# Kernel tuning notes

Hardware: AMD Instinct MI355X
Metric: run time of the kernel (lower is better)

The kernel has to match this reference:

```python
import jax, jax.numpy as jnp
import numpy as np

HIDDEN = 2048
HEAD_SIZE = 8
EXTRA = 4
NH = HEAD_SIZE * EXTRA          # 32 effective heads
D = HIDDEN // (HEAD_SIZE * 16)  # 16 per-head dim
PROJ = NH * D                   # 512
# NOTE: the torch module scales by att_size**-0.5 where att_size is the
# PRE-division value hidden//head_size//4 = 64, not the per-head dim D=16.
SCALE = (HIDDEN // HEAD_SIZE // EXTRA) ** -0.5


def _xavier(key, out_dim, in_dim):
    bound = float(np.sqrt(6.0 / (in_dim + out_dim)))
    return jax.random.uniform(key, (out_dim, in_dim), jnp.float32, -bound, bound)


def setup_inputs() -> dict:
    key = jax.random.key(0)
    ks = jax.random.split(key, 7)
    B, S = 2, 2048
    return {
        "q": jax.random.normal(ks[0], (B, S, HIDDEN), jnp.float32),
        "k": jax.random.normal(ks[1], (B, S, HIDDEN), jnp.float32),
        "v": jax.random.normal(ks[2], (B, S, HIDDEN), jnp.float32),
        "Wq": _xavier(ks[3], PROJ, HIDDEN),
        "Wk": _xavier(ks[4], PROJ, HIDDEN),
        "Wv": _xavier(ks[5], PROJ, HIDDEN),
        "Wo": _xavier(ks[6], HIDDEN, PROJ),
    }


def reference(q, k, v, Wq, Wk, Wv, Wo):
    B, S, _ = q.shape
    # projections (torch Linear: x @ W.T), reshape to [B,S,heads,d]
    qh = (q @ Wq.T).reshape(B, S, NH, D)
    kh = (k @ Wk.T).reshape(B, S, NH, D)
    vh = (v @ Wv.T).reshape(B, S, NH, D)
    scores = jnp.einsum("bshd,bthd->bhst", qh * SCALE, kh)  # [B,NH,S,S]
    attn = jax.nn.softmax(scores, axis=-1)
    out = jnp.einsum("bhst,bthd->bshd", attn, vh).reshape(B, S, PROJ)
    return out @ Wo.T  # [B,S,HIDDEN]
```

## Files before the change

kernel.cpp:

```cpp
#include <hip/hip_runtime.h>

#define HIDDEN 2048
#define NH 32
#define HD 16
#define PROJ 512
#define SEQ 2048

using f32x4    = __attribute__((ext_vector_type(4))) float;
using f32x2    = __attribute__((ext_vector_type(2))) float;
using bf16x8   = __attribute__((ext_vector_type(8))) __bf16;

__device__ __forceinline__ unsigned short f2bf(float x) {
  unsigned int u = __float_as_uint(x);
  u += 0x7FFFu + ((u >> 16) & 1u);
  return (unsigned short)(u >> 16);
}

__device__ __forceinline__ f32x4 mfma_bf16(bf16x8 a, bf16x8 b, f32x4 c) {
  return __builtin_amdgcn_mfma_f32_16x16x32_bf16(a, b, c, 0, 0, 0);
}

__device__ __forceinline__ f32x2 pk_add(f32x2 a, f32x2 b) {
  f32x2 d;
  asm("v_pk_add_f32 %0, %1, %2" : "=v"(d) : "v"(a), "v"(b));
  return d;
}

__device__ __forceinline__ unsigned int cvt_pk_bf16(float lo, float hi) {
  unsigned int d;
  asm("v_cvt_pk_bf16_f32 %0, %1, %2" : "=v"(d) : "v"(lo), "v"(hi));
  return d;
}

#define GLDS16(gptr, lptr)                                              \
  __builtin_amdgcn_global_load_lds(                                     \
      (const __attribute__((address_space(1))) unsigned int*)(gptr),    \
      (__attribute__((address_space(3))) unsigned int*)(lptr), 16, 0, 0)

__global__ __launch_bounds__(256)
void conv_kernel(const float* __restrict__ q, const float* __restrict__ k,
                 const float* __restrict__ v,
                 const float* __restrict__ Wq, const float* __restrict__ Wk,
                 const float* __restrict__ Wv, const float* __restrict__ Wo,
                 unsigned short* __restrict__ qb, unsigned short* __restrict__ kb,
                 unsigned short* __restrict__ vb,
                 unsigned short* __restrict__ Wqb, unsigned short* __restrict__ Wkb,
                 unsigned short* __restrict__ Wvb, unsigned short* __restrict__ Wob) {
  const int bid = blockIdx.x;
  const float* src;
  unsigned short* dst;
  size_t i;
  if (bid < 24576) {
    const int z = bid >> 13;
    const int off = bid & 8191;
    src = (z == 0) ? q : (z == 1) ? k : v;
    dst = (z == 0) ? qb : (z == 1) ? kb : vb;
    i = ((size_t)off * 256 + threadIdx.x) * 4;
  } else {
    const int r = bid - 24576;
    const int z = r >> 10;
    const int off = r & 1023;
    src = (z == 0) ? Wq : (z == 1) ? Wk : (z == 2) ? Wv : Wo;
    dst = (z == 0) ? Wqb : (z == 1) ? Wkb : (z == 2) ? Wvb : Wob;
    i = ((size_t)off * 256 + threadIdx.x) * 4;
  }
  f32x4 x = *(const f32x4*)(src + i);
  uint2 p;
  p.x = f2bf(x[0]) | ((unsigned)f2bf(x[1]) << 16);
  p.y = f2bf(x[2]) | ((unsigned)f2bf(x[3]) << 16);
  *(uint2*)(dst + i) = p;
}

__global__ __launch_bounds__(256)
void proj_kernel(const unsigned short* __restrict__ qb,
                 const unsigned short* __restrict__ kb,
                 const unsigned short* __restrict__ vb,
                 const unsigned short* __restrict__ Wqb,
                 const unsigned short* __restrict__ Wkb,
                 const unsigned short* __restrict__ Wvb,
                 unsigned short* __restrict__ qh, unsigned short* __restrict__ kh,
                 unsigned short* __restrict__ vt) {
  const int lin = blockIdx.x;
  const int e = lin & 7;
  const int t = lin >> 3;
  const int colt = t & 3;
  const int j = t >> 2;
  const int y = e + 8 * j;
  const int z = y >> 6;
  const int row0 = (y & 63) * 64;
  const int col0 = colt * 128;

  const unsigned short* A = (z == 0) ? qb : (z == 1) ? kb : vb;
  const unsigned short* Wb = (z == 0) ? Wqb : (z == 1) ? Wkb : Wvb;
  const float scale = (z == 0) ? 0.18033688011112042f  : 1.0f;

  __shared__ unsigned short As[64 * 32];
  __shared__ unsigned short Bs[128 * 32];

  const int tid = threadIdx.x;
  const int w = tid >> 6;
  const int lane = tid & 63;
  const int ln = lane & 15;
  const int qd = lane >> 4;
  const int wm = w >> 1, wn = w & 1;

  const int aM = tid >> 2;
  const int aG = (tid & 3) ^ (aM & 3);
  int bN[2], bG[2];
#pragma unroll
  for (int s = 0; s < 2; s++) {
    int L = s * 256 + tid;
    bN[s] = L >> 2;
    bG[s] = (L & 3) ^ (bN[s] & 3);
  }

  f32x4 acc[2][4];
#pragma unroll
  for (int mi = 0; mi < 2; mi++)
#pragma unroll
    for (int ni = 0; ni < 4; ni++) acc[mi][ni] = (f32x4){0.f, 0.f, 0.f, 0.f};

  for (int k0 = 0; k0 < HIDDEN; k0 += 32) {
    GLDS16(A + (size_t)(row0 + aM) * HIDDEN + k0 + aG * 8, &As[tid * 8]);
#pragma unroll
    for (int s = 0; s < 2; s++)
      GLDS16(Wb + (size_t)(col0 + bN[s]) * HIDDEN + k0 + bG[s] * 8,
             &Bs[(s * 256 + tid) * 8]);
    __syncthreads();

    bf16x8 af[2], bfv[4];
#pragma unroll
    for (int mi = 0; mi < 2; mi++) {
      int m = wm * 32 + mi * 16 + ln;
      af[mi] = *(const bf16x8*)&As[(m * 4 + (qd ^ (m & 3))) * 8];
    }
#pragma unroll
    for (int ni = 0; ni < 4; ni++) {
      int n = wn * 64 + ni * 16 + ln;
      bfv[ni] = *(const bf16x8*)&Bs[(n * 4 + (qd ^ (n & 3))) * 8];
    }
#pragma unroll
    for (int mi = 0; mi < 2; mi++)
#pragma unroll
      for (int ni = 0; ni < 4; ni++)
        acc[mi][ni] = mfma_bf16(af[mi], bfv[ni], acc[mi][ni]);
    __syncthreads();
  }

  if (z == 2) {
#pragma unroll
    for (int mi = 0; mi < 2; mi++)
#pragma unroll
      for (int ni = 0; ni < 4; ni++) {
        int h = (col0 + wn * 64 + ni * 16) >> 4;
        int grow0 = row0 + wm * 32 + mi * 16 + qd * 4;
        int b = grow0 >> 11, s0 = grow0 & 2047;
        uint2 o2;
        o2.x = f2bf(acc[mi][ni][0]) | ((unsigned)f2bf(acc[mi][ni][1]) << 16);
        o2.y = f2bf(acc[mi][ni][2]) | ((unsigned)f2bf(acc[mi][ni][3]) << 16);
        *(uint2*)&vt[((size_t)(b * NH + h) * HD + ln) * SEQ + s0] = o2;
      }
  } else {
    unsigned short* out = (z == 0) ? qh : kh;
#pragma unroll
    for (int mi = 0; mi < 2; mi++)
#pragma unroll
      for (int ni = 0; ni < 4; ni++) {
        int h = (col0 + wn * 64 + ni * 16) >> 4;
#pragma unroll
        for (int r = 0; r < 4; r++) {
          int grow = row0 + wm * 32 + mi * 16 + qd * 4 + r;
          int b = grow >> 11, s = grow & 2047;
          out[((size_t)(b * NH + h) * SEQ + s) * HD + ln] = f2bf(acc[mi][ni][r] * scale);
        }
      }
  }
}

__global__ __launch_bounds__(256, 4)
void flash_kernel(const unsigned short* __restrict__ qh,
                  const unsigned short* __restrict__ kh,
                  const unsigned short* __restrict__ vt,
                  unsigned short* __restrict__ attnb) {
  const int bh = blockIdx.x;
  const int b = bh >> 5, h = bh & 31;
  const int q0 = blockIdx.y * 128;
  const size_t hoff = (size_t)bh * SEQ * HD;
  const unsigned short* Qp = qh + hoff;
  const unsigned short* Kp = kh + hoff;
  const unsigned short* Vth = vt + hoff;

  __shared__ unsigned short Qs[128 * 16];
  __shared__ unsigned short Ks[2][128 * 16];
  __shared__ unsigned short Vts[2][256 * 8];
  __shared__ unsigned short Ps[4][32 * 40];
  __shared__ __align__(16) unsigned short Zz[8];

  const int tid = threadIdx.x;
  const int w = tid >> 6;
  const int lane = tid & 63;
  const int ln = lane & 15;
  const int qd = lane >> 4;
  const bool hiq = (qd >= 2);

  if (tid < 8) Zz[tid] = 0;

  const int vD = tid >> 4;
  const int vG = (tid & 15) ^ vD;

  const int qkOff = (tid >> 1) * 16 + (((tid & 1) ^ ((tid >> 3) & 1)) * 8);
  const int hsel = ((qd & 1) ^ ((ln >> 2) & 1)) * 8;

  GLDS16(Qp + (size_t)q0 * HD + qkOff, &Qs[tid * 8]);
  GLDS16(Kp + qkOff, &Ks[0][tid * 8]);
  GLDS16(Vth + (size_t)vD * SEQ + vG * 8, &Vts[0][tid * 8]);
  __syncthreads();

  bf16x8 aq[2];
#pragma unroll
  for (int ni = 0; ni < 2; ni++) {
    const unsigned short* src =
        hiq ? Zz : &Qs[(w * 32 + ni * 16 + ln) * 16 + hsel];
    aq[ni] = *(const bf16x8*)src;
  }

  f32x2 lsum2[2] = {{0.f, 0.f}, {0.f, 0.f}};
  f32x4 o_acc[2] = {{0.f, 0.f, 0.f, 0.f}, {0.f, 0.f, 0.f, 0.f}};
  unsigned short* Pw = &Ps[w][0];

  for (int t = 0; t < 16; t++) {
    const int buf = t & 1;
    if (t < 15) {
      GLDS16(Kp + (size_t)(t + 1) * 2048 + qkOff, &Ks[buf ^ 1][tid * 8]);
      GLDS16(Vth + (size_t)vD * SEQ + (t + 1) * 128 + vG * 8, &Vts[buf ^ 1][tid * 8]);
    }
    const unsigned short* Kb = &Ks[buf][0];
    const unsigned short* Vb = &Vts[buf][0];

#pragma unroll
    for (int c = 0; c < 4; c++) {
      f32x4 sc[2][2];
#pragma unroll
      for (int hf = 0; hf < 2; hf++) {
        int tile = c * 2 + hf;
        const unsigned short* asrc =
            hiq ? Zz : &Kb[(tile * 16 + ln) * 16 + hsel];
        bf16x8 ak = *(const bf16x8*)asrc;
#pragma unroll
        for (int ni = 0; ni < 2; ni++)
          sc[ni][hf] = mfma_bf16(ak, aq[ni], (f32x4){0.f, 0.f, 0.f, 0.f});
      }
      bf16x8 av = *(const bf16x8*)&Vb[(ln * 16 + ((c * 4 + qd) ^ ln)) * 8];

#pragma unroll
      for (int ni = 0; ni < 2; ni++) {
        float e0 = __builtin_amdgcn_exp2f(sc[ni][0][0]);
        float e1 = __builtin_amdgcn_exp2f(sc[ni][0][1]);
        float e2 = __builtin_amdgcn_exp2f(sc[ni][0][2]);
        float e3 = __builtin_amdgcn_exp2f(sc[ni][0][3]);
        float e4 = __builtin_amdgcn_exp2f(sc[ni][1][0]);
        float e5 = __builtin_amdgcn_exp2f(sc[ni][1][1]);
        float e6 = __builtin_amdgcn_exp2f(sc[ni][1][2]);
        float e7 = __builtin_amdgcn_exp2f(sc[ni][1][3]);
        f32x2 s01 = pk_add((f32x2){e0, e1}, (f32x2){e2, e3});
        f32x2 s23 = pk_add((f32x2){e4, e5}, (f32x2){e6, e7});
        lsum2[ni] = pk_add(lsum2[ni], pk_add(s01, s23));
        unsigned int d0 = cvt_pk_bf16(e0, e1);
        unsigned int d1 = cvt_pk_bf16(e2, e3);
        unsigned int d2 = cvt_pk_bf16(e4, e5);
        unsigned int d3 = cvt_pk_bf16(e6, e7);
        *(uint2*)&Pw[(ni * 16 + ln) * 40 + qd * 4] = make_uint2(d0, d1);
        *(uint2*)&Pw[(ni * 16 + ln) * 40 + 16 + qd * 4] = make_uint2(d2, d3);
      }

#pragma unroll
      for (int ni = 0; ni < 2; ni++) {
        bf16x8 bp = *(const bf16x8*)&Pw[(ni * 16 + ln) * 40 + qd * 8];
        o_acc[ni] = mfma_bf16(av, bp, o_acc[ni]);
      }
    }
    __syncthreads();
  }

#pragma unroll
  for (int ni = 0; ni < 2; ni++) {
    float l = lsum2[ni][0] + lsum2[ni][1];
    l += __shfl_xor(l, 16, 64);
    l += __shfl_xor(l, 32, 64);
    float invl = 1.0f / l;
    int s = q0 + w * 32 + ni * 16 + ln;
    f32x4 res = o_acc[ni] * invl;
    uint2 o2;
    o2.x = f2bf(res[0]) | ((unsigned)f2bf(res[1]) << 16);
    o2.y = f2bf(res[2]) | ((unsigned)f2bf(res[3]) << 16);
    *(uint2*)&attnb[((size_t)(b * SEQ + s)) * PROJ + h * HD + qd * 4] = o2;
  }
}

__global__ __launch_bounds__(256)
void out_kernel(const unsigned short* __restrict__ attnb,
                const unsigned short* __restrict__ Wob,
                float* __restrict__ out) {
  const int lin = blockIdx.x;
  const int e = lin & 7;
  const int t = lin >> 3;
  const int col0 = (e * 2 + (t & 1)) * 128;
  const int row0 = (t >> 1) * 64;

  __shared__ unsigned short As[64 * 32];
  __shared__ unsigned short Bs[128 * 32];

  const int tid = threadIdx.x;
  const int w = tid >> 6;
  const int lane = tid & 63;
  const int ln = lane & 15;
  const int qd = lane >> 4;
  const int wm = w >> 1, wn = w & 1;

  const int aM = tid >> 2;
  const int aG = (tid & 3) ^ (aM & 3);
  int bN[2], bG[2];
#pragma unroll
  for (int s = 0; s < 2; s++) {
    int L = s * 256 + tid;
    bN[s] = L >> 2;
    bG[s] = (L & 3) ^ (bN[s] & 3);
  }

  f32x4 acc[2][4];
#pragma unroll
  for (int mi = 0; mi < 2; mi++)
#pragma unroll
    for (int ni = 0; ni < 4; ni++) acc[mi][ni] = (f32x4){0.f, 0.f, 0.f, 0.f};

  for (int k0 = 0; k0 < PROJ; k0 += 32) {
    GLDS16(attnb + (size_t)(row0 + aM) * PROJ + k0 + aG * 8, &As[tid * 8]);
#pragma unroll
    for (int s = 0; s < 2; s++)
      GLDS16(Wob + (size_t)(col0 + bN[s]) * PROJ + k0 + bG[s] * 8,
             &Bs[(s * 256 + tid) * 8]);
    __syncthreads();

    bf16x8 af[2], bfv[4];
#pragma unroll
    for (int mi = 0; mi < 2; mi++) {
      int m = wm * 32 + mi * 16 + ln;
      af[mi] = *(const bf16x8*)&As[(m * 4 + (qd ^ (m & 3))) * 8];
    }
#pragma unroll
    for (int ni = 0; ni < 4; ni++) {
      int n = wn * 64 + ni * 16 + ln;
      bfv[ni] = *(const bf16x8*)&Bs[(n * 4 + (qd ^ (n & 3))) * 8];
    }
#pragma unroll
    for (int mi = 0; mi < 2; mi++)
#pragma unroll
      for (int ni = 0; ni < 4; ni++)
        acc[mi][ni] = mfma_bf16(bfv[ni], af[mi], acc[mi][ni]);
    __syncthreads();
  }

#pragma unroll
  for (int mi = 0; mi < 2; mi++) {
    int grow = row0 + wm * 32 + mi * 16 + ln;
#pragma unroll
    for (int ni = 0; ni < 4; ni++) {
      int gcol = col0 + wn * 64 + ni * 16 + qd * 4;
      *(f32x4*)&out[(size_t)grow * HIDDEN + gcol] = acc[mi][ni];
    }
  }
}

extern "C" void kernel_launch(void* const* d_in, const int* in_sizes, int n_in,
                              void* d_out, int out_size, void* d_ws, size_t ws_size,
                              hipStream_t stream) {
  const float* q  = (const float*)d_in[0];
  const float* k  = (const float*)d_in[1];
  const float* v  = (const float*)d_in[2];
  const float* Wq = (const float*)d_in[3];
  const float* Wk = (const float*)d_in[4];
  const float* Wv = (const float*)d_in[5];
  const float* Wo = (const float*)d_in[6];

  char* ws = (char*)d_ws;
  const size_t MB = 1024 * 1024;
  unsigned short* qh    = (unsigned short*)(ws);
  unsigned short* kh    = (unsigned short*)(ws + 4 * MB);
  unsigned short* vt    = (unsigned short*)(ws + 8 * MB);
  unsigned short* attnb = (unsigned short*)(ws + 12 * MB);
  unsigned short* Wqb   = (unsigned short*)(ws + 16 * MB);
  unsigned short* Wkb   = (unsigned short*)(ws + 18 * MB);
  unsigned short* Wvb   = (unsigned short*)(ws + 20 * MB);
  unsigned short* Wob   = (unsigned short*)(ws + 22 * MB);
  unsigned short* qb    = (unsigned short*)(ws + 24 * MB);
  unsigned short* kb    = (unsigned short*)(ws + 40 * MB);
  unsigned short* vb    = (unsigned short*)(ws + 56 * MB);

  conv_kernel<<<dim3(28672), dim3(256), 0, stream>>>(q, k, v, Wq, Wk, Wv, Wo,
                                                     qb, kb, vb, Wqb, Wkb, Wvb, Wob);
  proj_kernel<<<dim3(768), dim3(256), 0, stream>>>(qb, kb, vb, Wqb, Wkb, Wvb, qh, kh, vt);
  flash_kernel<<<dim3(64, 16), dim3(256), 0, stream>>>(qh, kh, vt, attnb);
  out_kernel<<<dim3(1024), dim3(256), 0, stream>>>(attnb, Wob, (float*)d_out);

  (void)in_sizes; (void)n_in; (void)out_size; (void)ws_size;
}
```

Baseline: 266.6 us.

## Fuse fp32-to-bf16 conversion into projection and output GEMM loads

Drops the separate conversion kernel. The projection and output GEMMs now load fp32 inputs and weights into registers, convert them to bf16 with v_cvt_pk_bf16, and store to LDS. The next K-slice is prefetched into registers after the barrier. The output GEMM tile also grows from 64 to 128 rows, halving its grid and reusing each Wo tile twice. This removes a full read and write of bf16 copies of q/k/v, but the main GEMM loop now reads twice the bytes from global memory, and LDS writes are synchronous rather than async global-to-LDS.

```diff
diff --git a/kernel.cpp b/kernel.cpp
--- a/kernel.cpp
+++ b/kernel.cpp
@@ -38,46 +38,10 @@
       (__attribute__((address_space(3))) unsigned int*)(lptr), 16, 0, 0)
 
 __global__ __launch_bounds__(256)
-void conv_kernel(const float* __restrict__ q, const float* __restrict__ k,
+void proj_kernel(const float* __restrict__ q, const float* __restrict__ k,
                  const float* __restrict__ v,
                  const float* __restrict__ Wq, const float* __restrict__ Wk,
-                 const float* __restrict__ Wv, const float* __restrict__ Wo,
-                 unsigned short* __restrict__ qb, unsigned short* __restrict__ kb,
-                 unsigned short* __restrict__ vb,
-                 unsigned short* __restrict__ Wqb, unsigned short* __restrict__ Wkb,
-                 unsigned short* __restrict__ Wvb, unsigned short* __restrict__ Wob) {
-  const int bid = blockIdx.x;
-  const float* src;
-  unsigned short* dst;
-  size_t i;
-  if (bid < 24576) {
-    const int z = bid >> 13;
-    const int off = bid & 8191;
-    src = (z == 0) ? q : (z == 1) ? k : v;
-    dst = (z == 0) ? qb : (z == 1) ? kb : vb;
-    i = ((size_t)off * 256 + threadIdx.x) * 4;
-  } else {
-    const int r = bid - 24576;
-    const int z = r >> 10;
-    const int off = r & 1023;
-    src = (z == 0) ? Wq : (z == 1) ? Wk : (z == 2) ? Wv : Wo;
-    dst = (z == 0) ? Wqb : (z == 1) ? Wkb : (z == 2) ? Wvb : Wob;
-    i = ((size_t)off * 256 + threadIdx.x) * 4;
-  }
-  f32x4 x = *(const f32x4*)(src + i);
-  uint2 p;
-  p.x = f2bf(x[0]) | ((unsigned)f2bf(x[1]) << 16);
-  p.y = f2bf(x[2]) | ((unsigned)f2bf(x[3]) << 16);
-  *(uint2*)(dst + i) = p;
-}
-
-__global__ __launch_bounds__(256)
-void proj_kernel(const unsigned short* __restrict__ qb,
-                 const unsigned short* __restrict__ kb,
-                 const unsigned short* __restrict__ vb,
-                 const unsigned short* __restrict__ Wqb,
-                 const unsigned short* __restrict__ Wkb,
-                 const unsigned short* __restrict__ Wvb,
+                 const float* __restrict__ Wv,
                  unsigned short* __restrict__ qh, unsigned short* __restrict__ kh,
                  unsigned short* __restrict__ vt) {
   const int lin = blockIdx.x;
@@ -90,8 +54,8 @@
   const int row0 = (y & 63) * 64;
   const int col0 = colt * 128;
 
-  const unsigned short* A = (z == 0) ? qb : (z == 1) ? kb : vb;
-  const unsigned short* Wb = (z == 0) ? Wqb : (z == 1) ? Wkb : Wvb;
+  const float* A = (z == 0) ? q : (z == 1) ? k : v;
+  const float* Wb = (z == 0) ? Wq : (z == 1) ? Wk : Wv;
   const float scale = (z == 0) ? 0.18033688011112042f  : 1.0f;
 
   __shared__ unsigned short As[64 * 32];
@@ -114,19 +78,52 @@
     bG[s] = (L & 3) ^ (bN[s] & 3);
   }
 
+  const float* Aptr  = A + (size_t)(row0 + aM) * HIDDEN + aG * 8;
+  const float* Bptr0 = Wb + (size_t)(col0 + bN[0]) * HIDDEN + bG[0] * 8;
+  const float* Bptr1 = Wb + (size_t)(col0 + bN[1]) * HIDDEN + bG[1] * 8;
+
   f32x4 acc[2][4];
 #pragma unroll
   for (int mi = 0; mi < 2; mi++)
 #pragma unroll
     for (int ni = 0; ni < 4; ni++) acc[mi][ni] = (f32x4){0.f, 0.f, 0.f, 0.f};
 
+  f32x4 ra0 = *(const f32x4*)(Aptr);
+  f32x4 ra1 = *(const f32x4*)(Aptr + 4);
+  f32x4 rb00 = *(const f32x4*)(Bptr0);
+  f32x4 rb01 = *(const f32x4*)(Bptr0 + 4);
+  f32x4 rb10 = *(const f32x4*)(Bptr1);
+  f32x4 rb11 = *(const f32x4*)(Bptr1 + 4);
+
   for (int k0 = 0; k0 < HIDDEN; k0 += 32) {
-    GLDS16(A + (size_t)(row0 + aM) * HIDDEN + k0 + aG * 8, &As[tid * 8]);
-#pragma unroll
-    for (int s = 0; s < 2; s++)
-      GLDS16(Wb + (size_t)(col0 + bN[s]) * HIDDEN + k0 + bG[s] * 8,
-             &Bs[(s * 256 + tid) * 8]);
+    uint4 wa;
+    wa.x = cvt_pk_bf16(ra0[0], ra0[1]);
+    wa.y = cvt_pk_bf16(ra0[2], ra0[3]);
+    wa.z = cvt_pk_bf16(ra1[0], ra1[1]);
+    wa.w = cvt_pk_bf16(ra1[2], ra1[3]);
+    *(uint4*)&As[tid * 8] = wa;
+    uint4 wb0;
+    wb0.x = cvt_pk_bf16(rb00[0], rb00[1]);
+    wb0.y = cvt_pk_bf16(rb00[2], rb00[3]);
+    wb0.z = cvt_pk_bf16(rb01[0], rb01[1]);
+    wb0.w = cvt_pk_bf16(rb01[2], rb01[3]);
+    *(uint4*)&Bs[tid * 8] = wb0;
+    uint4 wb1;
+    wb1.x = cvt_pk_bf16(rb10[0], rb10[1]);
+    wb1.y = cvt_pk_bf16(rb10[2], rb10[3]);
+    wb1.z = cvt_pk_bf16(rb11[0], rb11[1]);
+    wb1.w = cvt_pk_bf16(rb11[2], rb11[3]);
+    *(uint4*)&Bs[(256 + tid) * 8] = wb1;
     __syncthreads();
+
+    if (k0 + 32 < HIDDEN) {
+      ra0 = *(const f32x4*)(Aptr + k0 + 32);
+      ra1 = *(const f32x4*)(Aptr + k0 + 36);
+      rb00 = *(const f32x4*)(Bptr0 + k0 + 32);
+      rb01 = *(const f32x4*)(Bptr0 + k0 + 36);
+      rb10 = *(const f32x4*)(Bptr1 + k0 + 32);
+      rb11 = *(const f32x4*)(Bptr1 + k0 + 36);
+    }
 
     bf16x8 af[2], bfv[4];
 #pragma unroll
@@ -299,15 +296,15 @@
 
 __global__ __launch_bounds__(256)
 void out_kernel(const unsigned short* __restrict__ attnb,
-                const unsigned short* __restrict__ Wob,
+                const float* __restrict__ Wo,
                 float* __restrict__ out) {
   const int lin = blockIdx.x;
   const int e = lin & 7;
   const int t = lin >> 3;
   const int col0 = (e * 2 + (t & 1)) * 128;
-  const int row0 = (t >> 1) * 64;
-
-  __shared__ unsigned short As[64 * 32];
+  const int row0 = (t >> 1) * 128;
+
+  __shared__ unsigned short As[128 * 32];
   __shared__ unsigned short Bs[128 * 32];
 
   const int tid = threadIdx.x;
@@ -327,48 +324,80 @@
     bG[s] = (L & 3) ^ (bN[s] & 3);
   }
 
-  f32x4 acc[2][4];
-#pragma unroll
-  for (int mi = 0; mi < 2; mi++)
-#pragma unroll
-    for (int ni = 0; ni < 4; ni++) acc[mi][ni] = (f32x4){0.f, 0.f, 0.f, 0.f};
+  const float* Bptr0 = Wo + (size_t)(col0 + bN[0]) * PROJ + bG[0] * 8;
+  const float* Bptr1 = Wo + (size_t)(col0 + bN[1]) * PROJ + bG[1] * 8;
+
+  f32x4 acc[2][2][4];
+#pragma unroll
+  for (int s2 = 0; s2 < 2; s2++)
+#pragma unroll
+    for (int mi = 0; mi < 2; mi++)
+#pragma unroll
+      for (int ni = 0; ni < 4; ni++) acc[s2][mi][ni] = (f32x4){0.f, 0.f, 0.f, 0.f};
+
+  f32x4 rb00 = *(const f32x4*)(Bptr0);
+  f32x4 rb01 = *(const f32x4*)(Bptr0 + 4);
+  f32x4 rb10 = *(const f32x4*)(Bptr1);
+  f32x4 rb11 = *(const f32x4*)(Bptr1 + 4);
 
   for (int k0 = 0; k0 < PROJ; k0 += 32) {
     GLDS16(attnb + (size_t)(row0 + aM) * PROJ + k0 + aG * 8, &As[tid * 8]);
-#pragma unroll
-    for (int s = 0; s < 2; s++)
-      GLDS16(Wob + (size_t)(col0 + bN[s]) * PROJ + k0 + bG[s] * 8,
-             &Bs[(s * 256 + tid) * 8]);
+    GLDS16(attnb + (size_t)(row0 + 64 + aM) * PROJ + k0 + aG * 8, &As[(256 + tid) * 8]);
+    uint4 wb0;
+    wb0.x = cvt_pk_bf16(rb00[0], rb00[1]);
+    wb0.y = cvt_pk_bf16(rb00[2], rb00[3]);
+    wb0.z = cvt_pk_bf16(rb01[0], rb01[1]);
+    wb0.w = cvt_pk_bf16(rb01[2], rb01[3]);
+    *(uint4*)&Bs[tid * 8] = wb0;
+    uint4 wb1;
+    wb1.x = cvt_pk_bf16(rb10[0], rb10[1]);
+    wb1.y = cvt_pk_bf16(rb10[2], rb10[3]);
+    wb1.z = cvt_pk_bf16(rb11[0], rb11[1]);
+    wb1.w = cvt_pk_bf16(rb11[2], rb11[3]);
+    *(uint4*)&Bs[(256 + tid) * 8] = wb1;
     __syncthreads();
 
-    bf16x8 af[2], bfv[4];
-#pragma unroll
-    for (int mi = 0; mi < 2; mi++) {
-      int m = wm * 32 + mi * 16 + ln;
-      af[mi] = *(const bf16x8*)&As[(m * 4 + (qd ^ (m & 3))) * 8];
-    }
+    if (k0 + 32 < PROJ) {
+      rb00 = *(const f32x4*)(Bptr0 + k0 + 32);
+      rb01 = *(const f32x4*)(Bptr0 + k0 + 36);
+      rb10 = *(const f32x4*)(Bptr1 + k0 + 32);
+      rb11 = *(const f32x4*)(Bptr1 + k0 + 36);
+    }
+
+    bf16x8 af[2][2], bfv[4];
+#pragma unroll
+    for (int s2 = 0; s2 < 2; s2++)
+#pragma unroll
+      for (int mi = 0; mi < 2; mi++) {
+        int m = s2 * 64 + wm * 32 + mi * 16 + ln;
+        af[s2][mi] = *(const bf16x8*)&As[(m * 4 + (qd ^ (m & 3))) * 8];
+      }
 #pragma unroll
     for (int ni = 0; ni < 4; ni++) {
       int n = wn * 64 + ni * 16 + ln;
       bfv[ni] = *(const bf16x8*)&Bs[(n * 4 + (qd ^ (n & 3))) * 8];
     }
 #pragma unroll
-    for (int mi = 0; mi < 2; mi++)
-#pragma unroll
-      for (int ni = 0; ni < 4; ni++)
-        acc[mi][ni] = mfma_bf16(bfv[ni], af[mi], acc[mi][ni]);
+    for (int s2 = 0; s2 < 2; s2++)
+#pragma unroll
+      for (int mi = 0; mi < 2; mi++)
+#pragma unroll
+        for (int ni = 0; ni < 4; ni++)
+          acc[s2][mi][ni] = mfma_bf16(bfv[ni], af[s2][mi], acc[s2][mi][ni]);
     __syncthreads();
   }
 
 #pragma unroll
-  for (int mi = 0; mi < 2; mi++) {
-    int grow = row0 + wm * 32 + mi * 16 + ln;
-#pragma unroll
-    for (int ni = 0; ni < 4; ni++) {
-      int gcol = col0 + wn * 64 + ni * 16 + qd * 4;
-      *(f32x4*)&out[(size_t)grow * HIDDEN + gcol] = acc[mi][ni];
-    }
-  }
+  for (int s2 = 0; s2 < 2; s2++)
+#pragma unroll
+    for (int mi = 0; mi < 2; mi++) {
+      int grow = row0 + s2 * 64 + wm * 32 + mi * 16 + ln;
+#pragma unroll
+      for (int ni = 0; ni < 4; ni++) {
+        int gcol = col0 + wn * 64 + ni * 16 + qd * 4;
+        *(f32x4*)&out[(size_t)grow * HIDDEN + gcol] = acc[s2][mi][ni];
+      }
+    }
 }
 
 extern "C" void kernel_launch(void* const* d_in, const int* in_sizes, int n_in,
@@ -388,19 +417,10 @@
   unsigned short* kh    = (unsigned short*)(ws + 4 * MB);
   unsigned short* vt    = (unsigned short*)(ws + 8 * MB);
   unsigned short* attnb = (unsigned short*)(ws + 12 * MB);
-  unsigned short* Wqb   = (unsigned short*)(ws + 16 * MB);
-  unsigned short* Wkb   = (unsigned short*)(ws + 18 * MB);
-  unsigned short* Wvb   = (unsigned short*)(ws + 20 * MB);
-  unsigned short* Wob   = (unsigned short*)(ws + 22 * MB);
-  unsigned short* qb    = (unsigned short*)(ws + 24 * MB);
-  unsigned short* kb    = (unsigned short*)(ws + 40 * MB);
-  unsigned short* vb    = (unsigned short*)(ws + 56 * MB);
-
-  conv_kernel<<<dim3(28672), dim3(256), 0, stream>>>(q, k, v, Wq, Wk, Wv, Wo,
-                                                     qb, kb, vb, Wqb, Wkb, Wvb, Wob);
-  proj_kernel<<<dim3(768), dim3(256), 0, stream>>>(qb, kb, vb, Wqb, Wkb, Wvb, qh, kh, vt);
+
+  proj_kernel<<<dim3(768), dim3(256), 0, stream>>>(q, k, v, Wq, Wk, Wv, qh, kh, vt);
   flash_kernel<<<dim3(64, 16), dim3(256), 0, stream>>>(qh, kh, vt, attnb);
-  out_kernel<<<dim3(1024), dim3(256), 0, stream>>>(attnb, Wob, (float*)d_out);
+  out_kernel<<<dim3(512), dim3(256), 0, stream>>>(attnb, Wo, (float*)d_out);
 
   (void)in_sizes; (void)n_in; (void)out_size; (void)ws_size;
 }
```

Result: slower. 275.3 us (+3.3%).

## Double-buffer LDS tiles in projection and output GEMMs, enlarge output tile

Applied to the files above, without the earlier changes.

The projection and output GEMM kernels now hold two shared-memory buffers per operand. The next K-slice is prefetched while MFMAs run on the current slice, which overlaps global-to-LDS loads with compute and removes one barrier per iteration. The output kernel also doubles its row tile to 128, halving the grid to 512 blocks so each Wo tile loaded is reused across more rows. The cost is more LDS and more accumulator registers per block, which may lower occupancy.

```diff
diff --git a/kernel.cpp b/kernel.cpp
--- a/kernel.cpp
+++ b/kernel.cpp
@@ -94,8 +94,8 @@
   const unsigned short* Wb = (z == 0) ? Wqb : (z == 1) ? Wkb : Wvb;
   const float scale = (z == 0) ? 0.18033688011112042f  : 1.0f;
 
-  __shared__ unsigned short As[64 * 32];
-  __shared__ unsigned short Bs[128 * 32];
+  __shared__ unsigned short As[2][64 * 32];
+  __shared__ unsigned short Bs[2][128 * 32];
 
   const int tid = threadIdx.x;
   const int w = tid >> 6;
@@ -114,30 +114,39 @@
     bG[s] = (L & 3) ^ (bN[s] & 3);
   }
 
+  const unsigned short* Aptr  = A + (size_t)(row0 + aM) * HIDDEN + aG * 8;
+  const unsigned short* Bptr0 = Wb + (size_t)(col0 + bN[0]) * HIDDEN + bG[0] * 8;
+  const unsigned short* Bptr1 = Wb + (size_t)(col0 + bN[1]) * HIDDEN + bG[1] * 8;
+
   f32x4 acc[2][4];
 #pragma unroll
   for (int mi = 0; mi < 2; mi++)
 #pragma unroll
     for (int ni = 0; ni < 4; ni++) acc[mi][ni] = (f32x4){0.f, 0.f, 0.f, 0.f};
 
+  GLDS16(Aptr, &As[0][tid * 8]);
+  GLDS16(Bptr0, &Bs[0][tid * 8]);
+  GLDS16(Bptr1, &Bs[0][(256 + tid) * 8]);
+  __syncthreads();
+
   for (int k0 = 0; k0 < HIDDEN; k0 += 32) {
-    GLDS16(A + (size_t)(row0 + aM) * HIDDEN + k0 + aG * 8, &As[tid * 8]);
-#pragma unroll
-    for (int s = 0; s < 2; s++)
-      GLDS16(Wb + (size_t)(col0 + bN[s]) * HIDDEN + k0 + bG[s] * 8,
-             &Bs[(s * 256 + tid) * 8]);
-    __syncthreads();
+    const int cur = (k0 >> 5) & 1;
+    if (k0 + 32 < HIDDEN) {
+      GLDS16(Aptr + k0 + 32, &As[cur ^ 1][tid * 8]);
+      GLDS16(Bptr0 + k0 + 32, &Bs[cur ^ 1][tid * 8]);
+      GLDS16(Bptr1 + k0 + 32, &Bs[cur ^ 1][(256 + tid) * 8]);
+    }
 
     bf16x8 af[2], bfv[4];
 #pragma unroll
     for (int mi = 0; mi < 2; mi++) {
       int m = wm * 32 + mi * 16 + ln;
-      af[mi] = *(const bf16x8*)&As[(m * 4 + (qd ^ (m & 3))) * 8];
+      af[mi] = *(const bf16x8*)&As[cur][(m * 4 + (qd ^ (m & 3))) * 8];
     }
 #pragma unroll
     for (int ni = 0; ni < 4; ni++) {
       int n = wn * 64 + ni * 16 + ln;
-      bfv[ni] = *(const bf16x8*)&Bs[(n * 4 + (qd ^ (n & 3))) * 8];
+      bfv[ni] = *(const bf16x8*)&Bs[cur][(n * 4 + (qd ^ (n & 3))) * 8];
     }
 #pragma unroll
     for (int mi = 0; mi < 2; mi++)
@@ -305,10 +314,10 @@
   const int e = lin & 7;
   const int t = lin >> 3;
   const int col0 = (e * 2 + (t & 1)) * 128;
-  const int row0 = (t >> 1) * 64;
-
-  __shared__ unsigned short As[64 * 32];
-  __shared__ unsigned short Bs[128 * 32];
+  const int row0 = (t >> 1) * 128;
+
+  __shared__ unsigned short As[2][128 * 32];
+  __shared__ unsigned short Bs[2][128 * 32];
 
   const int tid = threadIdx.x;
   const int w = tid >> 6;
@@ -327,48 +336,68 @@
     bG[s] = (L & 3) ^ (bN[s] & 3);
   }
 
-  f32x4 acc[2][4];
-#pragma unroll
-  for (int mi = 0; mi < 2; mi++)
-#pragma unroll
-    for (int ni = 0; ni < 4; ni++) acc[mi][ni] = (f32x4){0.f, 0.f, 0.f, 0.f};
+  const unsigned short* Aptr0 = attnb + (size_t)(row0 + aM) * PROJ + aG * 8;
+  const unsigned short* Aptr1 = attnb + (size_t)(row0 + 64 + aM) * PROJ + aG * 8;
+  const unsigned short* Bptr0 = Wob + (size_t)(col0 + bN[0]) * PROJ + bG[0] * 8;
+  const unsigned short* Bptr1 = Wob + (size_t)(col0 + bN[1]) * PROJ + bG[1] * 8;
+
+  f32x4 acc[2][2][4];
+#pragma unroll
+  for (int s2 = 0; s2 < 2; s2++)
+#pragma unroll
+    for (int mi = 0; mi < 2; mi++)
+#pragma unroll
+      for (int ni = 0; ni < 4; ni++) acc[s2][mi][ni] = (f32x4){0.f, 0.f, 0.f, 0.f};
+
+  GLDS16(Aptr0, &As[0][tid * 8]);
+  GLDS16(Aptr1, &As[0][(256 + tid) * 8]);
+  GLDS16(Bptr0, &Bs[0][tid * 8]);
+  GLDS16(Bptr1, &Bs[0][(256 + tid) * 8]);
+  __syncthreads();
 
   for (int k0 = 0; k0 < PROJ; k0 += 32) {
-    GLDS16(attnb + (size_t)(row0 + aM) * PROJ + k0 + aG * 8, &As[tid * 8]);
-#pragma unroll
-    for (int s = 0; s < 2; s++)
-      GLDS16(Wob + (size_t)(col0 + bN[s]) * PROJ + k0 + bG[s] * 8,
-             &Bs[(s * 256 + tid) * 8]);
-    __syncthreads();
-
-    bf16x8 af[2], bfv[4];
-#pragma unroll
-    for (int mi = 0; mi < 2; mi++) {
-      int m = wm * 32 + mi * 16 + ln;
-      af[mi] = *(const bf16x8*)&As[(m * 4 + (qd ^ (m & 3))) * 8];
-    }
+    const int cur = (k0 >> 5) & 1;
+    if (k0 + 32 < PROJ) {
+      GLDS16(Aptr0 + k0 + 32, &As[cur ^ 1][tid * 8]);
+      GLDS16(Aptr1 + k0 + 32, &As[cur ^ 1][(256 + tid) * 8]);
+      GLDS16(Bptr0 + k0 + 32, &Bs[cur ^ 1][tid * 8]);
+      GLDS16(Bptr1 + k0 + 32, &Bs[cur ^ 1][(256 + tid) * 8]);
+    }
+
+    bf16x8 af[2][2], bfv[4];
+#pragma unroll
+    for (int s2 = 0; s2 < 2; s2++)
+#pragma unroll
+      for (int mi = 0; mi < 2; mi++) {
+        int m = s2 * 64 + wm * 32 + mi * 16 + ln;
+        af[s2][mi] = *(const bf16x8*)&As[cur][(m * 4 + (qd ^ (m & 3))) * 8];
+      }
 #pragma unroll
     for (int ni = 0; ni < 4; ni++) {
       int n = wn * 64 + ni * 16 + ln;
-      bfv[ni] = *(const bf16x8*)&Bs[(n * 4 + (qd ^ (n & 3))) * 8];
-    }
-#pragma unroll
-    for (int mi = 0; mi < 2; mi++)
-#pragma unroll
-      for (int ni = 0; ni < 4; ni++)
-        acc[mi][ni] = mfma_bf16(bfv[ni], af[mi], acc[mi][ni]);
+      bfv[ni] = *(const bf16x8*)&Bs[cur][(n * 4 + (qd ^ (n & 3))) * 8];
+    }
+#pragma unroll
+    for (int s2 = 0; s2 < 2; s2++)
+#pragma unroll
+      for (int mi = 0; mi < 2; mi++)
+#pragma unroll
+        for (int ni = 0; ni < 4; ni++)
+          acc[s2][mi][ni] = mfma_bf16(bfv[ni], af[s2][mi], acc[s2][mi][ni]);
     __syncthreads();
   }
 
 #pragma unroll
-  for (int mi = 0; mi < 2; mi++) {
-    int grow = row0 + wm * 32 + mi * 16 + ln;
-#pragma unroll
-    for (int ni = 0; ni < 4; ni++) {
-      int gcol = col0 + wn * 64 + ni * 16 + qd * 4;
-      *(f32x4*)&out[(size_t)grow * HIDDEN + gcol] = acc[mi][ni];
-    }
-  }
+  for (int s2 = 0; s2 < 2; s2++)
+#pragma unroll
+    for (int mi = 0; mi < 2; mi++) {
+      int grow = row0 + s2 * 64 + wm * 32 + mi * 16 + ln;
+#pragma unroll
+      for (int ni = 0; ni < 4; ni++) {
+        int gcol = col0 + wn * 64 + ni * 16 + qd * 4;
+        *(f32x4*)&out[(size_t)grow * HIDDEN + gcol] = acc[s2][mi][ni];
+      }
+    }
 }
 
 extern "C" void kernel_launch(void* const* d_in, const int* in_sizes, int n_in,
@@ -400,7 +429,7 @@
                                                      qb, kb, vb, Wqb, Wkb, Wvb, Wob);
   proj_kernel<<<dim3(768), dim3(256), 0, stream>>>(qb, kb, vb, Wqb, Wkb, Wvb, qh, kh, vt);
   flash_kernel<<<dim3(64, 16), dim3(256), 0, stream>>>(qh, kh, vt, attnb);
-  out_kernel<<<dim3(1024), dim3(256), 0, stream>>>(attnb, Wob, (float*)d_out);
+  out_kernel<<<dim3(512), dim3(256), 0, stream>>>(attnb, Wob, (float*)d_out);
 
   (void)in_sizes; (void)n_in; (void)out_size; (void)ws_size;
 }
```

Measured after the change: 266.6 us. Within noise of the previous version (-0.0%).
